# Performance work log

Measured on AMD Instinct MI355X. Metric: run time of the kernel, lower is better.

## Reference

```python
import jax, jax.numpy as jnp
import numpy as np

BN_EPS = 1e-5

def setup_inputs() -> dict:
    key = jax.random.key(0)
    ks = jax.random.split(key, 16)
    B, N = 64, 1024
    dims = [3, 64, 128, 256]
    H = 256
    inp = {"x": jax.random.normal(ks[0], (B, dims[0], N), dtype=jnp.float32)}
    for i in range(3):
        ci, co = dims[i], dims[i + 1]
        inp[f"w{i+1}"] = jax.random.normal(ks[1 + i], (co, ci), dtype=jnp.float32) * (1.0 / np.sqrt(ci))
        inp[f"b{i+1}"] = jnp.zeros((co,), dtype=jnp.float32)
        inp[f"g{i+1}"] = jnp.ones((co,), dtype=jnp.float32)
        inp[f"be{i+1}"] = jnp.zeros((co,), dtype=jnp.float32)
    inp["A"] = jnp.eye(H, dtype=jnp.float32) + 0.01 * jax.random.normal(ks[10], (H, H), dtype=jnp.float32)
    inp["Bm"] = 0.01 * jax.random.normal(ks[11], (H, dims[-1]), dtype=jnp.float32)
    inp["Cm"] = 0.01 * jax.random.normal(ks[12], (dims[-1], H), dtype=jnp.float32)
    return inp


def _conv_bn_relu(h, w, b, g, be):
    # h: [B, Cin, N]; 1x1 conv == channel matmul
    y = jnp.einsum('oi,bin->bon', w, h) + b[None, :, None]
    mu = jnp.mean(y, axis=(0, 2), keepdims=True)
    var = jnp.var(y, axis=(0, 2), keepdims=True)
    y = (y - mu) * jax.lax.rsqrt(var + BN_EPS)
    y = y * g[None, :, None] + be[None, :, None]
    return jax.nn.relu(y)


def reference(x, w1, b1, g1, be1, w2, b2, g2, be2, w3, b3, g3, be3, A, Bm, Cm):
    h = _conv_bn_relu(x, w1, b1, g1, be1)
    h = _conv_bn_relu(h, w2, b2, g2, be2)
    h = _conv_bn_relu(h, w3, b3, g3, be3)
    u = jnp.transpose(h, (0, 2, 1))  # [B, N, C]
    Bsz = u.shape[0]
    H = A.shape[0]
    A_norm = A / (jnp.linalg.norm(A, ord=2) + 1e-5)
    uB = u @ Bm.T  # precompute input projection: [B, N, H]

    def step(hstate, ut):
        hstate = jax.nn.relu(hstate @ A_norm.T + ut)
        return hstate, hstate @ Cm.T

    h0 = jnp.zeros((Bsz, H), dtype=x.dtype)
    _, ys = jax.lax.scan(step, h0, jnp.transpose(uB, (1, 0, 2)))  # ys: [N, B, Cout]
    y = jnp.transpose(ys, (1, 2, 0))  # [B, Cout, N]
    return y
```

## Files before the change

### kernel.cpp

```cpp
#include <hip/hip_runtime.h>

#define B_SZ 64
#define N_SZ 1024
#define C1   64
#define C2   128
#define C3   256
#define H_SZ 256

__global__ void k_btb(const float* __restrict__ A, float* __restrict__ B0) {
  int i = blockIdx.x;
  int j = threadIdx.x;
  float acc = 0.f;
  for (int k = 0; k < 256; ++k)
    acc = fmaf(A[k * 256 + i], A[k * 256 + j], acc);
  B0[i * 256 + j] = acc;
}

__global__ void k_bsq(const float* __restrict__ Bin, float* __restrict__ Bout) {
  __shared__ float diag[256];
  int i = blockIdx.x, j = threadIdx.x;
  diag[j] = Bin[j * 256 + j];
  __syncthreads();
  float tr = 0.f;
  for (int k = 0; k < 256; ++k) tr += diag[k];
  float inv = 1.0f / tr;
  float acc = 0.f;
  for (int k = 0; k < 256; ++k)
    acc = fmaf(Bin[i * 256 + k], Bin[k * 256 + j], acc);
  Bout[i * 256 + j] = acc * inv * inv;
}

__global__ void k_sfin(const float* __restrict__ Bf, const float* __restrict__ B0,
                       float* __restrict__ sinv) {
  __shared__ float v[256], w[256];
  __shared__ float red[256];
  __shared__ int redi[256];
  int t = threadIdx.x;
  red[t] = Bf[t * 256 + t];
  redi[t] = t;
  __syncthreads();
  for (int s = 128; s > 0; s >>= 1) {
    if (t < s) {
      if (red[t + s] > red[t]) { red[t] = red[t + s]; redi[t] = redi[t + s]; }
    }
    __syncthreads();
  }
  int jmax = redi[0];
  __syncthreads();
  v[t] = Bf[t * 256 + jmax];
  __syncthreads();
  float acc = 0.f;
  for (int k = 0; k < 256; ++k) acc = fmaf(B0[t * 256 + k], v[k], acc);
  w[t] = acc;
  __syncthreads();
  red[t] = v[t] * w[t];
  __syncthreads();
  for (int s = 128; s > 0; s >>= 1) { if (t < s) red[t] += red[t + s]; __syncthreads(); }
  float num = red[0];
  __syncthreads();
  red[t] = v[t] * v[t];
  __syncthreads();
  for (int s = 128; s > 0; s >>= 1) { if (t < s) red[t] += red[t + s]; __syncthreads(); }
  if (t == 0) {
    float lam = num / red[0];
    float sg = sqrtf(lam);
    *sinv = 1.0f / (sg + 1e-5f);
  }
}

__global__ void k_conv1(const float* __restrict__ x, const float* __restrict__ w,
                        const float* __restrict__ bias, float* __restrict__ y) {
  int b = blockIdx.x >> 2;
  int n = ((blockIdx.x & 3) << 8) + threadIdx.x;
  const float* xb = x + (size_t)b * 3 * N_SZ;
  float x0 = xb[n], x1 = xb[N_SZ + n], x2 = xb[2 * N_SZ + n];
  float* yb = y + (size_t)b * C1 * N_SZ;
#pragma unroll 4
  for (int o = 0; o < C1; ++o) {
    float r = fmaf(w[o * 3 + 0], x0,
              fmaf(w[o * 3 + 1], x1,
              fmaf(w[o * 3 + 2], x2, bias[o])));
    yb[(size_t)o * N_SZ + n] = r;
  }
}

__global__ void k_stats(const float* __restrict__ y, int C,
                        const float* __restrict__ g, const float* __restrict__ be,
                        float* __restrict__ coef) {
  int c = blockIdx.x;
  int t = threadIdx.x;
  float s1 = 0.f, s2 = 0.f;
  for (int b = 0; b < B_SZ; ++b) {
    const float4* p = (const float4*)(y + ((size_t)b * C + c) * N_SZ);
    float4 v = p[t];
    s1 += v.x + v.y + v.z + v.w;
    s2 += v.x * v.x + v.y * v.y + v.z * v.z + v.w * v.w;
  }
  __shared__ float r1[256], r2[256];
  r1[t] = s1; r2[t] = s2;
  __syncthreads();
  for (int s = 128; s > 0; s >>= 1) {
    if (t < s) { r1[t] += r1[t + s]; r2[t] += r2[t + s]; }
    __syncthreads();
  }
  if (t == 0) {
    const float M = (float)(B_SZ * N_SZ);
    float mu = r1[0] / M;
    float var = r2[0] / M - mu * mu;
    float sc = g[c] * rsqrtf(var + 1e-5f);
    coef[c] = sc;
    coef[C + c] = be[c] - mu * sc;
  }
}

template <int K, int CO>
__global__ void k_conv(const float* __restrict__ hin, const float* __restrict__ coef,
                       const float* __restrict__ w, const float* __restrict__ bias,
                       float* __restrict__ y) {
  __shared__ float wt[64][17];
  __shared__ float ht[16][65];
  int b = blockIdx.x, ot = blockIdx.y, nt = blockIdx.z;
  int t = threadIdx.x;
  int tx = t & 15, ty = t >> 4;
  float acc[4][4] = {};
  const float* hb = hin + (size_t)b * K * N_SZ + nt * 64;
  for (int k0 = 0; k0 < K; k0 += 16) {
    {
      int r = t >> 2, cc = (t & 3) * 4;
      const float* wp = w + (size_t)(ot * 64 + r) * K + k0 + cc;
      wt[r][cc + 0] = wp[0]; wt[r][cc + 1] = wp[1];
      wt[r][cc + 2] = wp[2]; wt[r][cc + 3] = wp[3];
    }
    {
      int r = t >> 4, cc = (t & 15) * 4;
      float sc = coef[k0 + r], sh = coef[K + k0 + r];
      const float* hp = hb + (size_t)(k0 + r) * N_SZ + cc;
      ht[r][cc + 0] = fmaxf(fmaf(hp[0], sc, sh), 0.f);
      ht[r][cc + 1] = fmaxf(fmaf(hp[1], sc, sh), 0.f);
      ht[r][cc + 2] = fmaxf(fmaf(hp[2], sc, sh), 0.f);
      ht[r][cc + 3] = fmaxf(fmaf(hp[3], sc, sh), 0.f);
    }
    __syncthreads();
#pragma unroll
    for (int k = 0; k < 16; ++k) {
      float hv[4], wv[4];
#pragma unroll
      for (int j = 0; j < 4; ++j) hv[j] = ht[k][tx * 4 + j];
#pragma unroll
      for (int i = 0; i < 4; ++i) wv[i] = wt[ty * 4 + i][k];
#pragma unroll
      for (int i = 0; i < 4; ++i)
#pragma unroll
        for (int j = 0; j < 4; ++j) acc[i][j] = fmaf(wv[i], hv[j], acc[i][j]);
    }
    __syncthreads();
  }
  float* yb = y + ((size_t)b * CO + ot * 64) * N_SZ + nt * 64;
#pragma unroll
  for (int i = 0; i < 4; ++i) {
    float bv = bias[ot * 64 + ty * 4 + i];
    float4 v;
    v.x = acc[i][0] + bv; v.y = acc[i][1] + bv;
    v.z = acc[i][2] + bv; v.w = acc[i][3] + bv;
    *(float4*)(yb + (size_t)(ty * 4 + i) * N_SZ + tx * 4) = v;
  }
}

__global__ void k_uB(const float* __restrict__ y3, const float* __restrict__ coef,
                     const float* __restrict__ Bm, float* __restrict__ uB) {
  __shared__ float xt[32][65];
  __shared__ float bt[64][33];
  int b = blockIdx.x, nt = blockIdx.y, htile = blockIdx.z;
  int t = threadIdx.x, tx = t & 15, ty = t >> 4;
  float acc[4][4] = {};
  const float* yb = y3 + (size_t)b * C3 * N_SZ + nt * 64;
  for (int c0 = 0; c0 < C3; c0 += 32) {
#pragma unroll
    for (int rr = 0; rr < 2; ++rr) {
      int r = (t >> 4) + rr * 16;
      int cidx = c0 + r;
      float sc = coef[cidx], sh = coef[C3 + cidx];
      int cc = (t & 15) * 4;
      const float* p = yb + (size_t)cidx * N_SZ + cc;
      xt[r][cc + 0] = fmaxf(fmaf(p[0], sc, sh), 0.f);
      xt[r][cc + 1] = fmaxf(fmaf(p[1], sc, sh), 0.f);
      xt[r][cc + 2] = fmaxf(fmaf(p[2], sc, sh), 0.f);
      xt[r][cc + 3] = fmaxf(fmaf(p[3], sc, sh), 0.f);
    }
#pragma unroll
    for (int rr = 0; rr < 2; ++rr) {
      int r = (t >> 3) + rr * 32;
      int cc = (t & 7) * 4;
      const float* p = Bm + (size_t)(htile * 64 + r) * H_SZ + c0 + cc;
      bt[r][cc + 0] = p[0]; bt[r][cc + 1] = p[1];
      bt[r][cc + 2] = p[2]; bt[r][cc + 3] = p[3];
    }
    __syncthreads();
#pragma unroll
    for (int k = 0; k < 32; ++k) {
      float xv[4], bv[4];
#pragma unroll
      for (int j = 0; j < 4; ++j) xv[j] = xt[k][ty * 4 + j];
#pragma unroll
      for (int i = 0; i < 4; ++i) bv[i] = bt[tx * 4 + i][k];
#pragma unroll
      for (int i = 0; i < 4; ++i)
#pragma unroll
        for (int j = 0; j < 4; ++j) acc[i][j] = fmaf(bv[i], xv[j], acc[i][j]);
    }
    __syncthreads();
  }
  float* ob = uB + (size_t)b * N_SZ * H_SZ;
#pragma unroll
  for (int j = 0; j < 4; ++j) {
    float4 v;
    v.x = acc[0][j]; v.y = acc[1][j]; v.z = acc[2][j]; v.w = acc[3][j];
    *(float4*)(ob + (size_t)(nt * 64 + ty * 4 + j) * H_SZ + htile * 64 + tx * 4) = v;
  }
}

__global__ __launch_bounds__(1024, 4) void k_scan(
    const float* __restrict__ A, const float* __restrict__ sinvp,
    const float* __restrict__ uB, float* __restrict__ hs) {
  __shared__ float h_lds[256];
  __shared__ float part[16][257];
  const int b = blockIdx.x;
  const int t = threadIdx.x;
  const int lane = t & 63;
  const int wv = t >> 6;
  const float sinv = *sinvp;
  float a0[16], a1[16], a2[16], a3[16];
  {
    const float* r0 = A + (size_t)(lane) * 256 + wv * 16;
    const float* r1 = A + (size_t)(lane + 64) * 256 + wv * 16;
    const float* r2 = A + (size_t)(lane + 128) * 256 + wv * 16;
    const float* r3 = A + (size_t)(lane + 192) * 256 + wv * 16;
#pragma unroll
    for (int j = 0; j < 16; ++j) {
      a0[j] = r0[j] * sinv; a1[j] = r1[j] * sinv;
      a2[j] = r2[j] * sinv; a3[j] = r3[j] * sinv;
    }
  }
  if (t < 256) h_lds[t] = 0.f;
  __syncthreads();
  const float* ub = uB + (size_t)b * N_SZ * H_SZ;
  float* ho = hs + (size_t)b * N_SZ * H_SZ;
  float u_cur = (t < 256) ? ub[t] : 0.f;
  for (int s = 0; s < N_SZ; ++s) {
    float u_next = 0.f;
    if (t < 256 && s + 1 < N_SZ) u_next = ub[(size_t)(s + 1) * H_SZ + t];
    const float4* hp = ((const float4*)h_lds) + wv * 4;
    float acc0 = 0.f, acc1 = 0.f, acc2 = 0.f, acc3 = 0.f;
#pragma unroll
    for (int q = 0; q < 4; ++q) {
      const float4 h4 = hp[q];
      const int jb = q * 4;
      acc0 = fmaf(a0[jb + 0], h4.x, acc0);
      acc0 = fmaf(a0[jb + 1], h4.y, acc0);
      acc0 = fmaf(a0[jb + 2], h4.z, acc0);
      acc0 = fmaf(a0[jb + 3], h4.w, acc0);
      acc1 = fmaf(a1[jb + 0], h4.x, acc1);
      acc1 = fmaf(a1[jb + 1], h4.y, acc1);
      acc1 = fmaf(a1[jb + 2], h4.z, acc1);
      acc1 = fmaf(a1[jb + 3], h4.w, acc1);
      acc2 = fmaf(a2[jb + 0], h4.x, acc2);
      acc2 = fmaf(a2[jb + 1], h4.y, acc2);
      acc2 = fmaf(a2[jb + 2], h4.z, acc2);
      acc2 = fmaf(a2[jb + 3], h4.w, acc2);
      acc3 = fmaf(a3[jb + 0], h4.x, acc3);
      acc3 = fmaf(a3[jb + 1], h4.y, acc3);
      acc3 = fmaf(a3[jb + 2], h4.z, acc3);
      acc3 = fmaf(a3[jb + 3], h4.w, acc3);
    }
    part[wv][lane] = acc0;
    part[wv][lane + 64] = acc1;
    part[wv][lane + 128] = acc2;
    part[wv][lane + 192] = acc3;
    __syncthreads();
    if (t < 256) {
      float p = u_cur;
#pragma unroll
      for (int q = 0; q < 16; ++q) p += part[q][t];
      p = fmaxf(p, 0.f);
      h_lds[t] = p;
      ho[(size_t)s * H_SZ + t] = p;
    }
    u_cur = u_next;
    __syncthreads();
  }
}

__global__ void k_ymm(const float* __restrict__ hs, const float* __restrict__ Cm,
                      float* __restrict__ y) {
  __shared__ float st[64][33];
  __shared__ float ct[64][33];
  int b = blockIdx.x, ot = blockIdx.y, nt = blockIdx.z;
  int t = threadIdx.x, tx = t & 15, ty = t >> 4;
  float acc[4][4] = {};
  const float* hb = hs + (size_t)b * N_SZ * H_SZ + (size_t)nt * 64 * H_SZ;
  for (int h0 = 0; h0 < H_SZ; h0 += 32) {
#pragma unroll
    for (int rr = 0; rr < 2; ++rr) {
      int r = (t >> 3) + rr * 32;
      int cc = (t & 7) * 4;
      const float* p = hb + (size_t)r * H_SZ + h0 + cc;
      st[r][cc + 0] = p[0]; st[r][cc + 1] = p[1];
      st[r][cc + 2] = p[2]; st[r][cc + 3] = p[3];
    }
#pragma unroll
    for (int rr = 0; rr < 2; ++rr) {
      int r = (t >> 3) + rr * 32;
      int cc = (t & 7) * 4;
      const float* p = Cm + (size_t)(ot * 64 + r) * H_SZ + h0 + cc;
      ct[r][cc + 0] = p[0]; ct[r][cc + 1] = p[1];
      ct[r][cc + 2] = p[2]; ct[r][cc + 3] = p[3];
    }
    __syncthreads();
#pragma unroll
    for (int k = 0; k < 32; ++k) {
      float sv[4], cv[4];
#pragma unroll
      for (int j = 0; j < 4; ++j) sv[j] = st[tx * 4 + j][k];
#pragma unroll
      for (int i = 0; i < 4; ++i) cv[i] = ct[ty * 4 + i][k];
#pragma unroll
      for (int i = 0; i < 4; ++i)
#pragma unroll
        for (int j = 0; j < 4; ++j) acc[i][j] = fmaf(cv[i], sv[j], acc[i][j]);
    }
    __syncthreads();
  }
  float* yb = y + ((size_t)b * C3 + ot * 64) * N_SZ + nt * 64;
#pragma unroll
  for (int i = 0; i < 4; ++i) {
    float4 v;
    v.x = acc[i][0]; v.y = acc[i][1]; v.z = acc[i][2]; v.w = acc[i][3];
    *(float4*)(yb + (size_t)(ty * 4 + i) * N_SZ + tx * 4) = v;
  }
}

extern "C" void kernel_launch(void* const* d_in, const int* in_sizes, int n_in,
                              void* d_out, int out_size, void* d_ws, size_t ws_size,
                              hipStream_t stream) {
  const float* x   = (const float*)d_in[0];
  const float* w1  = (const float*)d_in[1];
  const float* b1  = (const float*)d_in[2];
  const float* g1  = (const float*)d_in[3];
  const float* be1 = (const float*)d_in[4];
  const float* w2  = (const float*)d_in[5];
  const float* b2  = (const float*)d_in[6];
  const float* g2  = (const float*)d_in[7];
  const float* be2 = (const float*)d_in[8];
  const float* w3  = (const float*)d_in[9];
  const float* b3  = (const float*)d_in[10];
  const float* g3  = (const float*)d_in[11];
  const float* be3 = (const float*)d_in[12];
  const float* A   = (const float*)d_in[13];
  const float* Bm  = (const float*)d_in[14];
  const float* Cm  = (const float*)d_in[15];
  float* out = (float*)d_out;

  char* ws = (char*)d_ws;
  const size_t MB = 1024ull * 1024ull;
  float* y1 = (float*)(ws + 0);
  float* y2 = (float*)(ws + 16 * MB);
  float* y3 = (float*)(ws + 48 * MB);
  float* hs = (float*)(ws + 0);
  char* sp = ws + 112 * MB;
  float* B0 = (float*)(sp);
  float* P  = (float*)(sp + 256 * 1024);
  float* Q  = (float*)(sp + 512 * 1024);
  float* sinv  = (float*)(sp + 768 * 1024);
  float* coef1 = (float*)(sp + 768 * 1024 + 1024);
  float* coef2 = (float*)(sp + 768 * 1024 + 4096);
  float* coef3 = (float*)(sp + 768 * 1024 + 8192);

  k_btb<<<256, 256, 0, stream>>>(A, B0);
  {
    float* bufs[2] = {P, Q};
    const float* cur = B0;
    for (int it = 0; it < 12; ++it) {
      float* nxt = bufs[it & 1];
      k_bsq<<<256, 256, 0, stream>>>(cur, nxt);
      cur = nxt;
    }
    k_sfin<<<1, 256, 0, stream>>>(cur, B0, sinv);
  }

  k_conv1<<<dim3(B_SZ * 4), 256, 0, stream>>>(x, w1, b1, y1);
  k_stats<<<C1, 256, 0, stream>>>(y1, C1, g1, be1, coef1);
  k_conv<C1, C2><<<dim3(B_SZ, C2 / 64, N_SZ / 64), 256, 0, stream>>>(y1, coef1, w2, b2, y2);
  k_stats<<<C2, 256, 0, stream>>>(y2, C2, g2, be2, coef2);
  k_conv<C2, C3><<<dim3(B_SZ, C3 / 64, N_SZ / 64), 256, 0, stream>>>(y2, coef2, w3, b3, y3);
  k_stats<<<C3, 256, 0, stream>>>(y3, C3, g3, be3, coef3);

  k_uB<<<dim3(B_SZ, N_SZ / 64, H_SZ / 64), 256, 0, stream>>>(y3, coef3, Bm, out);

  k_scan<<<dim3(B_SZ), 1024, 0, stream>>>(A, sinv, out, hs);

  k_ymm<<<dim3(B_SZ, C3 / 64, N_SZ / 64), 256, 0, stream>>>(hs, Cm, out);
}
```

Measured before the change: 1.265 ms.

## Transpose GEMM LDS tiles for float4 reads and halve scan block size

The conv, uB and ymm GEMM kernels now store their weight and state tiles transposed in shared memory with a padding of 68. This lets the inner loop use float4 LDS reads in place of scalar strided reads, and the global loads are vectorised too. The scan kernel drops from 16 to 8 waves, so each thread holds 128 A entries in registers and the per-step cross-wave reduction is shorter. The risk is register pressure in the scan, which could cause spills, and some bank conflicts on the transposed shared-memory stores.

New measurement: 1.094 ms. 13.5% less time.

```diff
diff --git a/kernel.cpp b/kernel.cpp
--- a/kernel.cpp
+++ b/kernel.cpp
@@ -117,8 +117,8 @@
 __global__ void k_conv(const float* __restrict__ hin, const float* __restrict__ coef,
                        const float* __restrict__ w, const float* __restrict__ bias,
                        float* __restrict__ y) {
-  __shared__ float wt[64][17];
-  __shared__ float ht[16][65];
+  __shared__ float wt2[16][68];
+  __shared__ float ht[16][68];
   int b = blockIdx.x, ot = blockIdx.y, nt = blockIdx.z;
   int t = threadIdx.x;
   int tx = t & 15, ty = t >> 4;
@@ -127,31 +127,32 @@
   for (int k0 = 0; k0 < K; k0 += 16) {
     {
       int r = t >> 2, cc = (t & 3) * 4;
-      const float* wp = w + (size_t)(ot * 64 + r) * K + k0 + cc;
-      wt[r][cc + 0] = wp[0]; wt[r][cc + 1] = wp[1];
-      wt[r][cc + 2] = wp[2]; wt[r][cc + 3] = wp[3];
+      float4 v = *(const float4*)(w + (size_t)(ot * 64 + r) * K + k0 + cc);
+      wt2[cc + 0][r] = v.x; wt2[cc + 1][r] = v.y;
+      wt2[cc + 2][r] = v.z; wt2[cc + 3][r] = v.w;
     }
     {
       int r = t >> 4, cc = (t & 15) * 4;
       float sc = coef[k0 + r], sh = coef[K + k0 + r];
       const float* hp = hb + (size_t)(k0 + r) * N_SZ + cc;
-      ht[r][cc + 0] = fmaxf(fmaf(hp[0], sc, sh), 0.f);
-      ht[r][cc + 1] = fmaxf(fmaf(hp[1], sc, sh), 0.f);
-      ht[r][cc + 2] = fmaxf(fmaf(hp[2], sc, sh), 0.f);
-      ht[r][cc + 3] = fmaxf(fmaf(hp[3], sc, sh), 0.f);
+      float4 v;
+      v.x = fmaxf(fmaf(hp[0], sc, sh), 0.f);
+      v.y = fmaxf(fmaf(hp[1], sc, sh), 0.f);
+      v.z = fmaxf(fmaf(hp[2], sc, sh), 0.f);
+      v.w = fmaxf(fmaf(hp[3], sc, sh), 0.f);
+      *(float4*)&ht[r][cc] = v;
     }
     __syncthreads();
 #pragma unroll
     for (int k = 0; k < 16; ++k) {
-      float hv[4], wv[4];
-#pragma unroll
-      for (int j = 0; j < 4; ++j) hv[j] = ht[k][tx * 4 + j];
-#pragma unroll
-      for (int i = 0; i < 4; ++i) wv[i] = wt[ty * 4 + i][k];
+      float4 hv = *(const float4*)&ht[k][tx * 4];
+      float4 wv = *(const float4*)&wt2[k][ty * 4];
+      float hvv[4] = {hv.x, hv.y, hv.z, hv.w};
+      float wvv[4] = {wv.x, wv.y, wv.z, wv.w};
 #pragma unroll
       for (int i = 0; i < 4; ++i)
 #pragma unroll
-        for (int j = 0; j < 4; ++j) acc[i][j] = fmaf(wv[i], hv[j], acc[i][j]);
+        for (int j = 0; j < 4; ++j) acc[i][j] = fmaf(wvv[i], hvv[j], acc[i][j]);
     }
     __syncthreads();
   }
@@ -168,8 +169,8 @@
 
 __global__ void k_uB(const float* __restrict__ y3, const float* __restrict__ coef,
                      const float* __restrict__ Bm, float* __restrict__ uB) {
-  __shared__ float xt[32][65];
-  __shared__ float bt[64][33];
+  __shared__ float xt[32][68];
+  __shared__ float bt2[32][68];
   int b = blockIdx.x, nt = blockIdx.y, htile = blockIdx.z;
   int t = threadIdx.x, tx = t & 15, ty = t >> 4;
   float acc[4][4] = {};
@@ -182,31 +183,32 @@
       float sc = coef[cidx], sh = coef[C3 + cidx];
       int cc = (t & 15) * 4;
       const float* p = yb + (size_t)cidx * N_SZ + cc;
-      xt[r][cc + 0] = fmaxf(fmaf(p[0], sc, sh), 0.f);
-      xt[r][cc + 1] = fmaxf(fmaf(p[1], sc, sh), 0.f);
-      xt[r][cc + 2] = fmaxf(fmaf(p[2], sc, sh), 0.f);
-      xt[r][cc + 3] = fmaxf(fmaf(p[3], sc, sh), 0.f);
+      float4 v;
+      v.x = fmaxf(fmaf(p[0], sc, sh), 0.f);
+      v.y = fmaxf(fmaf(p[1], sc, sh), 0.f);
+      v.z = fmaxf(fmaf(p[2], sc, sh), 0.f);
+      v.w = fmaxf(fmaf(p[3], sc, sh), 0.f);
+      *(float4*)&xt[r][cc] = v;
     }
 #pragma unroll
     for (int rr = 0; rr < 2; ++rr) {
       int r = (t >> 3) + rr * 32;
       int cc = (t & 7) * 4;
-      const float* p = Bm + (size_t)(htile * 64 + r) * H_SZ + c0 + cc;
-      bt[r][cc + 0] = p[0]; bt[r][cc + 1] = p[1];
-      bt[r][cc + 2] = p[2]; bt[r][cc + 3] = p[3];
+      float4 v = *(const float4*)(Bm + (size_t)(htile * 64 + r) * H_SZ + c0 + cc);
+      bt2[cc + 0][r] = v.x; bt2[cc + 1][r] = v.y;
+      bt2[cc + 2][r] = v.z; bt2[cc + 3][r] = v.w;
     }
     __syncthreads();
 #pragma unroll
     for (int k = 0; k < 32; ++k) {
-      float xv[4], bv[4];
-#pragma unroll
-      for (int j = 0; j < 4; ++j) xv[j] = xt[k][ty * 4 + j];
-#pragma unroll
-      for (int i = 0; i < 4; ++i) bv[i] = bt[tx * 4 + i][k];
+      float4 xv = *(const float4*)&xt[k][ty * 4];
+      float4 bv = *(const float4*)&bt2[k][tx * 4];
+      float xvv[4] = {xv.x, xv.y, xv.z, xv.w};
+      float bvv[4] = {bv.x, bv.y, bv.z, bv.w};
 #pragma unroll
       for (int i = 0; i < 4; ++i)
 #pragma unroll
-        for (int j = 0; j < 4; ++j) acc[i][j] = fmaf(bv[i], xv[j], acc[i][j]);
+        for (int j = 0; j < 4; ++j) acc[i][j] = fmaf(bvv[i], xvv[j], acc[i][j]);
     }
     __syncthreads();
   }
@@ -219,27 +221,22 @@
   }
 }
 
-__global__ __launch_bounds__(1024, 4) void k_scan(
+__global__ __launch_bounds__(512, 2) void k_scan(
     const float* __restrict__ A, const float* __restrict__ sinvp,
     const float* __restrict__ uB, float* __restrict__ hs) {
   __shared__ float h_lds[256];
-  __shared__ float part[16][257];
+  __shared__ float part[8][256];
   const int b = blockIdx.x;
   const int t = threadIdx.x;
   const int lane = t & 63;
   const int wv = t >> 6;
   const float sinv = *sinvp;
-  float a0[16], a1[16], a2[16], a3[16];
-  {
-    const float* r0 = A + (size_t)(lane) * 256 + wv * 16;
-    const float* r1 = A + (size_t)(lane + 64) * 256 + wv * 16;
-    const float* r2 = A + (size_t)(lane + 128) * 256 + wv * 16;
-    const float* r3 = A + (size_t)(lane + 192) * 256 + wv * 16;
-#pragma unroll
-    for (int j = 0; j < 16; ++j) {
-      a0[j] = r0[j] * sinv; a1[j] = r1[j] * sinv;
-      a2[j] = r2[j] * sinv; a3[j] = r3[j] * sinv;
-    }
+  float areg[4][32];
+#pragma unroll
+  for (int k = 0; k < 4; ++k) {
+    const float* r = A + (size_t)(lane + 64 * k) * 256 + wv * 32;
+#pragma unroll
+    for (int j = 0; j < 32; ++j) areg[k][j] = r[j] * sinv;
   }
   if (t < 256) h_lds[t] = 0.f;
   __syncthreads();
@@ -249,38 +246,28 @@
   for (int s = 0; s < N_SZ; ++s) {
     float u_next = 0.f;
     if (t < 256 && s + 1 < N_SZ) u_next = ub[(size_t)(s + 1) * H_SZ + t];
-    const float4* hp = ((const float4*)h_lds) + wv * 4;
-    float acc0 = 0.f, acc1 = 0.f, acc2 = 0.f, acc3 = 0.f;
-#pragma unroll
-    for (int q = 0; q < 4; ++q) {
+    const float4* hp = ((const float4*)h_lds) + wv * 8;
+    float acc[4] = {0.f, 0.f, 0.f, 0.f};
+#pragma unroll
+    for (int q = 0; q < 8; ++q) {
       const float4 h4 = hp[q];
-      const int jb = q * 4;
-      acc0 = fmaf(a0[jb + 0], h4.x, acc0);
-      acc0 = fmaf(a0[jb + 1], h4.y, acc0);
-      acc0 = fmaf(a0[jb + 2], h4.z, acc0);
-      acc0 = fmaf(a0[jb + 3], h4.w, acc0);
-      acc1 = fmaf(a1[jb + 0], h4.x, acc1);
-      acc1 = fmaf(a1[jb + 1], h4.y, acc1);
-      acc1 = fmaf(a1[jb + 2], h4.z, acc1);
-      acc1 = fmaf(a1[jb + 3], h4.w, acc1);
-      acc2 = fmaf(a2[jb + 0], h4.x, acc2);
-      acc2 = fmaf(a2[jb + 1], h4.y, acc2);
-      acc2 = fmaf(a2[jb + 2], h4.z, acc2);
-      acc2 = fmaf(a2[jb + 3], h4.w, acc2);
-      acc3 = fmaf(a3[jb + 0], h4.x, acc3);
-      acc3 = fmaf(a3[jb + 1], h4.y, acc3);
-      acc3 = fmaf(a3[jb + 2], h4.z, acc3);
-      acc3 = fmaf(a3[jb + 3], h4.w, acc3);
-    }
-    part[wv][lane] = acc0;
-    part[wv][lane + 64] = acc1;
-    part[wv][lane + 128] = acc2;
-    part[wv][lane + 192] = acc3;
+#pragma unroll
+      for (int k = 0; k < 4; ++k) {
+        acc[k] = fmaf(areg[k][q * 4 + 0], h4.x, acc[k]);
+        acc[k] = fmaf(areg[k][q * 4 + 1], h4.y, acc[k]);
+        acc[k] = fmaf(areg[k][q * 4 + 2], h4.z, acc[k]);
+        acc[k] = fmaf(areg[k][q * 4 + 3], h4.w, acc[k]);
+      }
+    }
+    part[wv][lane] = acc[0];
+    part[wv][lane + 64] = acc[1];
+    part[wv][lane + 128] = acc[2];
+    part[wv][lane + 192] = acc[3];
     __syncthreads();
     if (t < 256) {
       float p = u_cur;
 #pragma unroll
-      for (int q = 0; q < 16; ++q) p += part[q][t];
+      for (int c = 0; c < 8; ++c) p += part[c][t];
       p = fmaxf(p, 0.f);
       h_lds[t] = p;
       ho[(size_t)s * H_SZ + t] = p;
@@ -292,8 +279,8 @@
 
 __global__ void k_ymm(const float* __restrict__ hs, const float* __restrict__ Cm,
                       float* __restrict__ y) {
-  __shared__ float st[64][33];
-  __shared__ float ct[64][33];
+  __shared__ float st2[32][68];
+  __shared__ float ct2[32][68];
   int b = blockIdx.x, ot = blockIdx.y, nt = blockIdx.z;
   int t = threadIdx.x, tx = t & 15, ty = t >> 4;
   float acc[4][4] = {};
@@ -303,30 +290,29 @@
     for (int rr = 0; rr < 2; ++rr) {
       int r = (t >> 3) + rr * 32;
       int cc = (t & 7) * 4;
-      const float* p = hb + (size_t)r * H_SZ + h0 + cc;
-      st[r][cc + 0] = p[0]; st[r][cc + 1] = p[1];
-      st[r][cc + 2] = p[2]; st[r][cc + 3] = p[3];
+      float4 v = *(const float4*)(hb + (size_t)r * H_SZ + h0 + cc);
+      st2[cc + 0][r] = v.x; st2[cc + 1][r] = v.y;
+      st2[cc + 2][r] = v.z; st2[cc + 3][r] = v.w;
     }
 #pragma unroll
     for (int rr = 0; rr < 2; ++rr) {
       int r = (t >> 3) + rr * 32;
       int cc = (t & 7) * 4;
-      const float* p = Cm + (size_t)(ot * 64 + r) * H_SZ + h0 + cc;
-      ct[r][cc + 0] = p[0]; ct[r][cc + 1] = p[1];
-      ct[r][cc + 2] = p[2]; ct[r][cc + 3] = p[3];
+      float4 v = *(const float4*)(Cm + (size_t)(ot * 64 + r) * H_SZ + h0 + cc);
+      ct2[cc + 0][r] = v.x; ct2[cc + 1][r] = v.y;
+      ct2[cc + 2][r] = v.z; ct2[cc + 3][r] = v.w;
     }
     __syncthreads();
 #pragma unroll
     for (int k = 0; k < 32; ++k) {
-      float sv[4], cv[4];
-#pragma unroll
-      for (int j = 0; j < 4; ++j) sv[j] = st[tx * 4 + j][k];
-#pragma unroll
-      for (int i = 0; i < 4; ++i) cv[i] = ct[ty * 4 + i][k];
+      float4 sv = *(const float4*)&st2[k][tx * 4];
+      float4 cv = *(const float4*)&ct2[k][ty * 4];
+      float svv[4] = {sv.x, sv.y, sv.z, sv.w};
+      float cvv[4] = {cv.x, cv.y, cv.z, cv.w};
 #pragma unroll
       for (int i = 0; i < 4; ++i)
 #pragma unroll
-        for (int j = 0; j < 4; ++j) acc[i][j] = fmaf(cv[i], sv[j], acc[i][j]);
+        for (int j = 0; j < 4; ++j) acc[i][j] = fmaf(cvv[i], svv[j], acc[i][j]);
     }
     __syncthreads();
   }
@@ -396,7 +382,7 @@
 
   k_uB<<<dim3(B_SZ, N_SZ / 64, H_SZ / 64), 256, 0, stream>>>(y3, coef3, Bm, out);
 
-  k_scan<<<dim3(B_SZ), 1024, 0, stream>>>(A, sinv, out, hs);
+  k_scan<<<dim3(B_SZ), 512, 0, stream>>>(A, sinv, out, hs);
 
   k_ymm<<<dim3(B_SZ, C3 / 64, N_SZ / 64), 256, 0, stream>>>(hs, Cm, out);
 }
```
